# Kernel optimization log

Hardware: AMD Instinct MI355X
Metric: run time of the kernel (lower is better)

The kernel has to match this reference:

```python
import jax, jax.numpy as jnp
import numpy as np

N_NODES = 100000
N_EDGES = 3200000
NUM_FEATURES = 256
HIDDEN = 16
NUM_CLASSES = 40


def gcn_conv(x, edge_index, W, b, num_nodes):
    """PyG GCNConv: linear -> add self-loops -> symmetric deg norm -> scatter-add -> bias."""
    x = x @ W  # [N, out]
    loop = jnp.arange(num_nodes)
    src = jnp.concatenate([edge_index[0], loop])  # messages flow src -> dst
    dst = jnp.concatenate([edge_index[1], loop])
    # degree of target nodes (with self-loops)
    deg = jax.ops.segment_sum(jnp.ones_like(dst, dtype=x.dtype), dst,
                              num_segments=num_nodes)
    dinv = jnp.where(deg > 0, jax.lax.rsqrt(deg), 0.0)
    norm = dinv[src] * dinv[dst]  # [E+N]
    out = jax.ops.segment_sum(x[src] * norm[:, None], dst,
                              num_segments=num_nodes)
    return out + b


def setup_inputs() -> dict:
    key = jax.random.key(0)
    k1, k2, k3, k4 = jax.random.split(key, 4)
    x = jax.random.normal(k1, (N_NODES, NUM_FEATURES), dtype=jnp.float32)
    edge_index = jax.random.randint(k2, (2, N_EDGES), 0, N_NODES, dtype=jnp.int64)
    W1 = jax.random.normal(k3, (NUM_FEATURES, HIDDEN), dtype=jnp.float32) / np.sqrt(NUM_FEATURES)
    b1 = jnp.zeros((HIDDEN,), dtype=jnp.float32)
    W2 = jax.random.normal(k4, (HIDDEN, NUM_CLASSES), dtype=jnp.float32) / np.sqrt(HIDDEN)
    b2 = jnp.zeros((NUM_CLASSES,), dtype=jnp.float32)
    return {"x": x, "edge_index": edge_index, "W1": W1, "b1": b1, "W2": W2, "b2": b2}


def reference(x, edge_index, W1, b1, W2, b2):
    h = jax.nn.relu(gcn_conv(x, edge_index, W1, b1, N_NODES))
    return gcn_conv(h, edge_index, W2, b2, N_NODES)
```

## Files before the change

### kernel.cpp

```cpp
#include <hip/hip_runtime.h>
#include <hip/hip_fp16.h>

#define N_NODES   100000
#define N_EDGES   3200000
#define F_IN      256
#define HID       16
#define NCLS      40

#define CHUNK     8192
#define NCHK      ((N_EDGES + CHUNK - 1) / CHUNK)
#define GRID1     392
#define B2SHIFT   9
#define NB2       ((N_NODES + 511) >> B2SHIFT)
#define BCAP      17408

__global__ __launch_bounds__(128) void k1_all(const int* __restrict__ ei,
                                              const float* __restrict__ x,
                                              const float* __restrict__ W1,
                                              int* __restrict__ gcnt,
                                              int* __restrict__ buf,
                                              __half* __restrict__ y1h) {
    __shared__ float W1s[F_IN * HID];
    int* h   = (int*)W1s;
    int* cur = ((int*)W1s) + 256;
    int blk = blockIdx.x, t = threadIdx.x;

    if (blk < NCHK) {
        for (int j = t; j < NB2; j += 128) h[j] = 0;
        __syncthreads();
        int e0 = blk * CHUNK;
        int eN = min(CHUNK, N_EDGES - e0);
        const int4* d4 = (const int4*)(ei + N_EDGES + e0);
        const int4* s4 = (const int4*)(ei + e0);
        for (int i = t; i < (eN >> 2); i += 128) {
            int4 d = d4[i];
            atomicAdd(&h[d.x >> B2SHIFT], 1);
            atomicAdd(&h[d.y >> B2SHIFT], 1);
            atomicAdd(&h[d.z >> B2SHIFT], 1);
            atomicAdd(&h[d.w >> B2SHIFT], 1);
        }
        __syncthreads();
        for (int j = t; j < NB2; j += 128)
            cur[j] = j * BCAP + atomicAdd(&gcnt[j], h[j]);
        __syncthreads();
        for (int i = t; i < (eN >> 2); i += 128) {
            int4 d = d4[i], s = s4[i];
            int p0 = atomicAdd(&cur[d.x >> B2SHIFT], 1); buf[p0] = ((d.x & 511) << 17) | s.x;
            int p1 = atomicAdd(&cur[d.y >> B2SHIFT], 1); buf[p1] = ((d.y & 511) << 17) | s.y;
            int p2 = atomicAdd(&cur[d.z >> B2SHIFT], 1); buf[p2] = ((d.z & 511) << 17) | s.z;
            int p3 = atomicAdd(&cur[d.w >> B2SHIFT], 1); buf[p3] = ((d.w & 511) << 17) | s.w;
        }
        __syncthreads();
    }

    for (int i = t; i < F_IN * HID; i += 128) W1s[i] = W1[i];
    __syncthreads();

    int n0 = blk * 256 + t;
    int n1 = n0 + 128;
    if (n0 >= N_NODES) return;
    bool v1 = (n1 < N_NODES);

    const float4* xr0 = (const float4*)(x + (size_t)n0 * F_IN);
    const float4* xr1 = (const float4*)(x + (size_t)(v1 ? n1 : n0) * F_IN);
    float acc0[HID], acc1[HID];
    #pragma unroll
    for (int j = 0; j < HID; j++) { acc0[j] = 0.f; acc1[j] = 0.f; }

    #pragma unroll 2
    for (int k4 = 0; k4 < F_IN / 4; k4++) {
        float4 xa = xr0[k4];
        float4 xb = xr1[k4];
        int k = k4 * 4;
        #pragma unroll
        for (int hh = 0; hh < HID; hh++) {
            float w0 = W1s[(k + 0) * HID + hh];
            float w1 = W1s[(k + 1) * HID + hh];
            float w2 = W1s[(k + 2) * HID + hh];
            float w3 = W1s[(k + 3) * HID + hh];
            acc0[hh] += xa.x * w0 + xa.y * w1 + xa.z * w2 + xa.w * w3;
            acc1[hh] += xb.x * w0 + xb.y * w1 + xb.z * w2 + xb.w * w3;
        }
    }
    {
        __half2 hp[8];
        #pragma unroll
        for (int j = 0; j < 8; j++)
            hp[j] = __float22half2_rn(make_float2(acc0[2 * j], acc0[2 * j + 1]));
        float4* o = (float4*)(y1h + (size_t)n0 * HID);
        o[0] = ((float4*)hp)[0];
        o[1] = ((float4*)hp)[1];
    }
    if (v1) {
        __half2 hp[8];
        #pragma unroll
        for (int j = 0; j < 8; j++)
            hp[j] = __float22half2_rn(make_float2(acc1[2 * j], acc1[2 * j + 1]));
        float4* o = (float4*)(y1h + (size_t)n1 * HID);
        o[0] = ((float4*)hp)[0];
        o[1] = ((float4*)hp)[1];
    }
}

__global__ __launch_bounds__(512) void k3_build(const int* __restrict__ buf,
                                               const int* __restrict__ gcnt,
                                               int* __restrict__ rowptr,
                                               float* __restrict__ dinv,
                                               int* __restrict__ csr_src,
                                               __half* __restrict__ y1h) {
    __shared__ int lbuf[BCAP];
    __shared__ int hist[512], offs[512], cur[512];
    __shared__ int sc[256];
    __shared__ int s_base, s_cnt;
    int b = blockIdx.x, t = threadIdx.x;

    int cntv = 0;
    if (t < 256) { cntv = (t < NB2) ? gcnt[t] : 0; sc[t] = cntv; }
    hist[t] = 0;
    __syncthreads();
    for (int off = 1; off < 256; off <<= 1) {
        int u = 0;
        if (t < 256 && t >= off) u = sc[t - off];
        __syncthreads();
        if (t < 256) sc[t] += u;
        __syncthreads();
    }
    if (t == b) { s_base = sc[b] - cntv; s_cnt = cntv; }
    __syncthreads();
    int base = s_base, cnt = s_cnt;
    int src0 = b * BCAP;

    for (int i = t; i < cnt; i += 512) {
        int v = buf[src0 + i];
        if (i < BCAP) lbuf[i] = v;
        atomicAdd(&hist[v >> 17], 1);
    }
    __syncthreads();
    int v = hist[t];
    offs[t] = v;
    __syncthreads();
    for (int off = 1; off < 512; off <<= 1) {
        int u = (t >= off) ? offs[t - off] : 0;
        __syncthreads();
        offs[t] += u;
        __syncthreads();
    }
    int ex = offs[t] - v;
    int n = (b << B2SHIFT) + t;
    if (n < N_NODES) {
        rowptr[n] = base + ex;
        float dv = rsqrtf((float)(v + 1));
        dinv[n] = dv;
        float4* yr = (float4*)(y1h + (size_t)n * HID);
        float4 a = yr[0], bq = yr[1];
        __half2* ah = (__half2*)&a;
        __half2* bh = (__half2*)&bq;
        #pragma unroll
        for (int j = 0; j < 4; j++) {
            float2 fa = __half22float2(ah[j]);
            float2 fb = __half22float2(bh[j]);
            ah[j] = __float22half2_rn(make_float2(fa.x * dv, fa.y * dv));
            bh[j] = __float22half2_rn(make_float2(fb.x * dv, fb.y * dv));
        }
        yr[0] = a;
        yr[1] = bq;
    }
    if (b == 0 && t == 0) rowptr[N_NODES] = N_EDGES;
    cur[t] = ex;
    __syncthreads();
    for (int i = t; i < cnt; i += 512) {
        int p = (i < BCAP) ? lbuf[i] : buf[src0 + i];
        int pos = atomicAdd(&cur[p >> 17], 1);
        csr_src[base + pos] = p & 0x1FFFF;
    }
}

__device__ __forceinline__ void acc_row(const float4* __restrict__ tab, int s, float* acc) {
    float4 v0 = tab[(size_t)s * 2 + 0];
    float4 v1 = tab[(size_t)s * 2 + 1];
    const __half2* a0 = (const __half2*)&v0;
    const __half2* a1 = (const __half2*)&v1;
    #pragma unroll
    for (int j = 0; j < 4; j++) {
        float2 f0 = __half22float2(a0[j]);
        float2 f1 = __half22float2(a1[j]);
        acc[2 * j]         += f0.x;
        acc[2 * j + 1]     += f0.y;
        acc[8 + 2 * j]     += f1.x;
        acc[8 + 2 * j + 1] += f1.y;
    }
}

__device__ __forceinline__ void acc_row2(const float4* __restrict__ tab, int s0, int s1, float* acc) {
    float4 v0 = tab[(size_t)s0 * 2 + 0];
    float4 v1 = tab[(size_t)s0 * 2 + 1];
    float4 v2 = tab[(size_t)s1 * 2 + 0];
    float4 v3 = tab[(size_t)s1 * 2 + 1];
    const __half2* a0 = (const __half2*)&v0;
    const __half2* a1 = (const __half2*)&v1;
    const __half2* b0 = (const __half2*)&v2;
    const __half2* b1 = (const __half2*)&v3;
    #pragma unroll
    for (int j = 0; j < 4; j++) {
        float2 f0 = __half22float2(a0[j]);
        float2 f1 = __half22float2(a1[j]);
        float2 g0 = __half22float2(b0[j]);
        float2 g1 = __half22float2(b1[j]);
        acc[2 * j]         += f0.x + g0.x;
        acc[2 * j + 1]     += f0.y + g0.y;
        acc[8 + 2 * j]     += f1.x + g1.x;
        acc[8 + 2 * j + 1] += f1.y + g1.y;
    }
}

__global__ __launch_bounds__(256) void gather1_kernel(const int* __restrict__ rowptr,
                                                      const int* __restrict__ csr_src,
                                                      const __half* __restrict__ y1h,
                                                      const float* __restrict__ b1,
                                                      const float* __restrict__ dinv,
                                                      __half* __restrict__ zh) {
    int n   = blockIdx.x * 64 + (threadIdx.x >> 2);
    int sub = threadIdx.x & 3;
    if (n >= N_NODES) return;
    const float4* tab = (const float4*)y1h;
    int beg = rowptr[n], end = rowptr[n + 1];
    float acc[16];
    #pragma unroll
    for (int i = 0; i < 16; i++) acc[i] = 0.f;
    if (sub == 0) acc_row(tab, n, acc);
    int e = beg + sub;
    for (; e + 4 < end; e += 8)
        acc_row2(tab, csr_src[e], csr_src[e + 4], acc);
    if (e < end) acc_row(tab, csr_src[e], acc);
    #pragma unroll
    for (int m = 1; m < 4; m <<= 1) {
        #pragma unroll
        for (int i = 0; i < 16; i++) acc[i] += __shfl_xor(acc[i], m, 4);
    }
    if (sub < 2) {
        float dvn = dinv[n];
        const float4* b1q = (const float4*)b1;
        float4 ba = b1q[sub * 2], bb = b1q[sub * 2 + 1];
        float bv[8] = {ba.x, ba.y, ba.z, ba.w, bb.x, bb.y, bb.z, bb.w};
        __half2 outp[4];
        #pragma unroll
        for (int j = 0; j < 4; j++) {
            float2 r;
            r.x = fmaxf(dvn * acc[sub * 8 + 2 * j]     + bv[2 * j],     0.f) * dvn;
            r.y = fmaxf(dvn * acc[sub * 8 + 2 * j + 1] + bv[2 * j + 1], 0.f) * dvn;
            outp[j] = __float22half2_rn(r);
        }
        *(float4*)(zh + (size_t)n * HID + sub * 8) = *(float4*)outp;
    }
}

__global__ __launch_bounds__(256) void gather2_kernel(const int* __restrict__ rowptr,
                                                      const int* __restrict__ csr_src,
                                                      const __half* __restrict__ zh,
                                                      const float* __restrict__ W2,
                                                      const float* __restrict__ b2,
                                                      const float* __restrict__ dinv,
                                                      float* __restrict__ out) {
    __shared__ float W2s[HID * NCLS];
    __shared__ float b2s[NCLS];
    int t = threadIdx.x;
    for (int i = t; i < HID * NCLS; i += 256) W2s[i] = W2[i];
    if (t < NCLS) b2s[t] = b2[t];
    __syncthreads();

    int n   = blockIdx.x * 64 + (t >> 2);
    int sub = t & 3;
    if (n >= N_NODES) return;
    const float4* tab = (const float4*)zh;
    int beg = rowptr[n], end = rowptr[n + 1];
    float acc[16];
    #pragma unroll
    for (int i = 0; i < 16; i++) acc[i] = 0.f;
    if (sub == 0) acc_row(tab, n, acc);
    int e = beg + sub;
    for (; e + 4 < end; e += 8)
        acc_row2(tab, csr_src[e], csr_src[e + 4], acc);
    if (e < end) acc_row(tab, csr_src[e], acc);
    #pragma unroll
    for (int m = 1; m < 4; m <<= 1) {
        #pragma unroll
        for (int i = 0; i < 16; i++) acc[i] += __shfl_xor(acc[i], m, 4);
    }
    float dv = dinv[n];
    int c0 = sub * 10;
    float o[10];
    #pragma unroll
    for (int j = 0; j < 10; j++) o[j] = 0.f;
    #pragma unroll
    for (int h = 0; h < HID; h++) {
        float a = acc[h];
        const float* w = &W2s[h * NCLS + c0];
        #pragma unroll
        for (int j = 0; j < 10; j++) o[j] += a * w[j];
    }
    float* op = out + (size_t)n * NCLS + c0;
    #pragma unroll
    for (int j = 0; j < 5; j++) {
        float2 r = make_float2(dv * o[2 * j]     + b2s[c0 + 2 * j],
                               dv * o[2 * j + 1] + b2s[c0 + 2 * j + 1]);
        *(float2*)(op + 2 * j) = r;
    }
}

extern "C" void kernel_launch(void* const* d_in, const int* in_sizes, int n_in,
                              void* d_out, int out_size, void* d_ws, size_t ws_size,
                              hipStream_t stream) {
    const float* x   = (const float*)d_in[0];
    const int*   ei  = (const int*)  d_in[1];
    const float* W1  = (const float*)d_in[2];
    const float* b1  = (const float*)d_in[3];
    const float* W2  = (const float*)d_in[4];
    const float* b2  = (const float*)d_in[5];
    float* out = (float*)d_out;

    char* ws = (char*)d_ws;
    size_t off = 0;
    int*   gcnt = (int*)(ws + off); off += (size_t)NB2 * 4;
    off = (off + 15) & ~(size_t)15;
    int*    rowptr  = (int*)   (ws + off); off += (size_t)(N_NODES + 1) * 4;
    off = (off + 15) & ~(size_t)15;
    float*  dinv    = (float*) (ws + off); off += (size_t)N_NODES * 4;
    int*    csr_src = (int*)   (ws + off); off += (size_t)N_EDGES * 4;
    int*    buf     = (int*)   (ws + off); off += (size_t)NB2 * BCAP * 4;
    __half* y1h     = (__half*)(ws + off); off += (size_t)N_NODES * HID * 2;
    __half* zh      = (__half*)(ws + off); off += (size_t)N_NODES * HID * 2;

    hipMemsetAsync(gcnt, 0, (size_t)NB2 * 4, stream);
    k1_all   <<<GRID1, 128, 0, stream>>>(ei, x, W1, gcnt, buf, y1h);
    k3_build <<<NB2, 512, 0, stream>>>(buf, gcnt, rowptr, dinv, csr_src, y1h);
    gather1_kernel<<<(N_NODES + 63) / 64, 256, 0, stream>>>(rowptr, csr_src, y1h, b1, dinv, zh);
    gather2_kernel<<<(N_NODES + 63) / 64, 256, 0, stream>>>(rowptr, csr_src, zh, W2, b2, dinv, out);
}
```

Baseline: 333.3 us.

## Restructure GCN pipeline: global-atomic degrees, fuse CSR build with layer-1 gather

Degree counting moves to global atomics inside the GEMM kernel. Binning and the dinv scaling of y1 move into a new second kernel. The CSR build kernel now also does the layer-1 gather, using a per-bucket sorted source list held in LDS, so the separate gather1 launch and the dinv array go away. Layer 2 recomputes dinv from the rowptr difference. In exchange, the edge list is read an extra time, 3.2M global atomics hit deg, and the fused gather runs one thread per node with only 196 blocks, which may be poorly balanced.

```diff
diff --git a/kernel.cpp b/kernel.cpp
--- a/kernel.cpp
+++ b/kernel.cpp
@@ -7,57 +7,37 @@
 #define HID       16
 #define NCLS      40
 
-#define CHUNK     8192
-#define NCHK      ((N_EDGES + CHUNK - 1) / CHUNK)
-#define GRID1     392
+#define CHUNK     16384
+#define NBLK      ((N_EDGES + CHUNK - 1) / CHUNK)
 #define B2SHIFT   9
 #define NB2       ((N_NODES + 511) >> B2SHIFT)
 #define BCAP      17408
 
-__global__ __launch_bounds__(128) void k1_all(const int* __restrict__ ei,
-                                              const float* __restrict__ x,
-                                              const float* __restrict__ W1,
-                                              int* __restrict__ gcnt,
-                                              int* __restrict__ buf,
-                                              __half* __restrict__ y1h) {
+__global__ __launch_bounds__(256) void k1_gemm_deg(const int* __restrict__ ei,
+                                                   const float* __restrict__ x,
+                                                   const float* __restrict__ W1,
+                                                   int* __restrict__ deg,
+                                                   __half* __restrict__ y1h) {
     __shared__ float W1s[F_IN * HID];
-    int* h   = (int*)W1s;
-    int* cur = ((int*)W1s) + 256;
     int blk = blockIdx.x, t = threadIdx.x;
 
-    if (blk < NCHK) {
-        for (int j = t; j < NB2; j += 128) h[j] = 0;
-        __syncthreads();
-        int e0 = blk * CHUNK;
-        int eN = min(CHUNK, N_EDGES - e0);
-        const int4* d4 = (const int4*)(ei + N_EDGES + e0);
-        const int4* s4 = (const int4*)(ei + e0);
-        for (int i = t; i < (eN >> 2); i += 128) {
-            int4 d = d4[i];
-            atomicAdd(&h[d.x >> B2SHIFT], 1);
-            atomicAdd(&h[d.y >> B2SHIFT], 1);
-            atomicAdd(&h[d.z >> B2SHIFT], 1);
-            atomicAdd(&h[d.w >> B2SHIFT], 1);
-        }
-        __syncthreads();
-        for (int j = t; j < NB2; j += 128)
-            cur[j] = j * BCAP + atomicAdd(&gcnt[j], h[j]);
-        __syncthreads();
-        for (int i = t; i < (eN >> 2); i += 128) {
-            int4 d = d4[i], s = s4[i];
-            int p0 = atomicAdd(&cur[d.x >> B2SHIFT], 1); buf[p0] = ((d.x & 511) << 17) | s.x;
-            int p1 = atomicAdd(&cur[d.y >> B2SHIFT], 1); buf[p1] = ((d.y & 511) << 17) | s.y;
-            int p2 = atomicAdd(&cur[d.z >> B2SHIFT], 1); buf[p2] = ((d.z & 511) << 17) | s.z;
-            int p3 = atomicAdd(&cur[d.w >> B2SHIFT], 1); buf[p3] = ((d.w & 511) << 17) | s.w;
-        }
-        __syncthreads();
-    }
-
-    for (int i = t; i < F_IN * HID; i += 128) W1s[i] = W1[i];
-    __syncthreads();
-
-    int n0 = blk * 256 + t;
-    int n1 = n0 + 128;
+    #pragma unroll
+    for (int i = 0; i < (F_IN * HID) / 256; i++) W1s[t + i * 256] = W1[t + i * 256];
+
+    int e0 = blk * CHUNK;
+    int eN = min(CHUNK, N_EDGES - e0);
+    const int4* d4 = (const int4*)(ei + N_EDGES + e0);
+    for (int i = t; i < (eN >> 2); i += 256) {
+        int4 d = d4[i];
+        atomicAdd(&deg[d.x], 1);
+        atomicAdd(&deg[d.y], 1);
+        atomicAdd(&deg[d.z], 1);
+        atomicAdd(&deg[d.w], 1);
+    }
+    __syncthreads();
+
+    int n0 = blk * 512 + t;
+    int n1 = n0 + 256;
     if (n0 >= N_NODES) return;
     bool v1 = (n1 < N_NODES);
 
@@ -102,55 +82,17 @@
     }
 }
 
-__global__ __launch_bounds__(512) void k3_build(const int* __restrict__ buf,
-                                               const int* __restrict__ gcnt,
-                                               int* __restrict__ rowptr,
-                                               float* __restrict__ dinv,
-                                               int* __restrict__ csr_src,
-                                               __half* __restrict__ y1h) {
-    __shared__ int lbuf[BCAP];
-    __shared__ int hist[512], offs[512], cur[512];
-    __shared__ int sc[256];
-    __shared__ int s_base, s_cnt;
-    int b = blockIdx.x, t = threadIdx.x;
-
-    int cntv = 0;
-    if (t < 256) { cntv = (t < NB2) ? gcnt[t] : 0; sc[t] = cntv; }
-    hist[t] = 0;
-    __syncthreads();
-    for (int off = 1; off < 256; off <<= 1) {
-        int u = 0;
-        if (t < 256 && t >= off) u = sc[t - off];
-        __syncthreads();
-        if (t < 256) sc[t] += u;
-        __syncthreads();
-    }
-    if (t == b) { s_base = sc[b] - cntv; s_cnt = cntv; }
-    __syncthreads();
-    int base = s_base, cnt = s_cnt;
-    int src0 = b * BCAP;
-
-    for (int i = t; i < cnt; i += 512) {
-        int v = buf[src0 + i];
-        if (i < BCAP) lbuf[i] = v;
-        atomicAdd(&hist[v >> 17], 1);
-    }
-    __syncthreads();
-    int v = hist[t];
-    offs[t] = v;
-    __syncthreads();
-    for (int off = 1; off < 512; off <<= 1) {
-        int u = (t >= off) ? offs[t - off] : 0;
-        __syncthreads();
-        offs[t] += u;
-        __syncthreads();
-    }
-    int ex = offs[t] - v;
-    int n = (b << B2SHIFT) + t;
+__global__ __launch_bounds__(512) void k2_scale_bin(const int* __restrict__ ei,
+                                                    const int* __restrict__ deg,
+                                                    __half* __restrict__ y1h,
+                                                    int* __restrict__ gcnt,
+                                                    int* __restrict__ buf) {
+    __shared__ int h[NB2], cur[NB2];
+    int blk = blockIdx.x, t = threadIdx.x;
+
+    int n = blk * 512 + t;
     if (n < N_NODES) {
-        rowptr[n] = base + ex;
-        float dv = rsqrtf((float)(v + 1));
-        dinv[n] = dv;
+        float dv = rsqrtf((float)(deg[n] + 1));
         float4* yr = (float4*)(y1h + (size_t)n * HID);
         float4 a = yr[0], bq = yr[1];
         __half2* ah = (__half2*)&a;
@@ -165,13 +107,30 @@
         yr[0] = a;
         yr[1] = bq;
     }
-    if (b == 0 && t == 0) rowptr[N_NODES] = N_EDGES;
-    cur[t] = ex;
-    __syncthreads();
-    for (int i = t; i < cnt; i += 512) {
-        int p = (i < BCAP) ? lbuf[i] : buf[src0 + i];
-        int pos = atomicAdd(&cur[p >> 17], 1);
-        csr_src[base + pos] = p & 0x1FFFF;
+
+    for (int j = t; j < NB2; j += 512) h[j] = 0;
+    __syncthreads();
+    int e0 = blk * CHUNK;
+    int eN = min(CHUNK, N_EDGES - e0);
+    const int4* s4 = (const int4*)(ei + e0);
+    const int4* d4 = (const int4*)(ei + N_EDGES + e0);
+    for (int i = t; i < (eN >> 2); i += 512) {
+        int4 d = d4[i];
+        atomicAdd(&h[d.x >> B2SHIFT], 1);
+        atomicAdd(&h[d.y >> B2SHIFT], 1);
+        atomicAdd(&h[d.z >> B2SHIFT], 1);
+        atomicAdd(&h[d.w >> B2SHIFT], 1);
+    }
+    __syncthreads();
+    for (int j = t; j < NB2; j += 512)
+        cur[j] = j * BCAP + atomicAdd(&gcnt[j], h[j]);
+    __syncthreads();
+    for (int i = t; i < (eN >> 2); i += 512) {
+        int4 d = d4[i], s = s4[i];
+        int p0 = atomicAdd(&cur[d.x >> B2SHIFT], 1); buf[p0] = ((d.x & 511) << 17) | s.x;
+        int p1 = atomicAdd(&cur[d.y >> B2SHIFT], 1); buf[p1] = ((d.y & 511) << 17) | s.y;
+        int p2 = atomicAdd(&cur[d.z >> B2SHIFT], 1); buf[p2] = ((d.z & 511) << 17) | s.z;
+        int p3 = atomicAdd(&cur[d.w >> B2SHIFT], 1); buf[p3] = ((d.w & 511) << 17) | s.w;
     }
 }
 
@@ -213,16 +172,106 @@
     }
 }
 
-__global__ __launch_bounds__(256) void gather1_kernel(const int* __restrict__ rowptr,
+__global__ __launch_bounds__(512) void k3_build_gather(const int* __restrict__ buf,
+                                                       const int* __restrict__ gcnt,
+                                                       int* __restrict__ rowptr,
+                                                       int* __restrict__ csr_src,
+                                                       const __half* __restrict__ y1h,
+                                                       const float* __restrict__ b1,
+                                                       __half* __restrict__ zh) {
+    __shared__ int lsorted[BCAP];
+    __shared__ int hist[512], offs[512], cur[512];
+    __shared__ int sc[256];
+    __shared__ float b1s[HID];
+    __shared__ int s_base, s_cnt;
+    int b = blockIdx.x, t = threadIdx.x;
+
+    if (t < HID) b1s[t] = b1[t];
+    int cntv = 0;
+    if (t < 256) { cntv = (t < NB2) ? gcnt[t] : 0; sc[t] = cntv; }
+    hist[t] = 0;
+    __syncthreads();
+    for (int off = 1; off < 256; off <<= 1) {
+        int u = 0;
+        if (t < 256 && t >= off) u = sc[t - off];
+        __syncthreads();
+        if (t < 256) sc[t] += u;
+        __syncthreads();
+    }
+    if (t == b) { s_base = sc[b] - cntv; s_cnt = cntv; }
+    __syncthreads();
+    int base = s_base, cnt = s_cnt;
+    int src0 = b * BCAP;
+
+    for (int i = t; i < cnt; i += 512)
+        atomicAdd(&hist[buf[src0 + i] >> 17], 1);
+    __syncthreads();
+    int v = hist[t];
+    offs[t] = v;
+    __syncthreads();
+    for (int off = 1; off < 512; off <<= 1) {
+        int u = (t >= off) ? offs[t - off] : 0;
+        __syncthreads();
+        offs[t] += u;
+        __syncthreads();
+    }
+    int ex = offs[t] - v;
+    int n = (b << B2SHIFT) + t;
+    if (n < N_NODES) rowptr[n] = base + ex;
+    if (b == 0 && t == 0) rowptr[N_NODES] = N_EDGES;
+    cur[t] = ex;
+    __syncthreads();
+    for (int i = t; i < cnt; i += 512) {
+        int p = buf[src0 + i];
+        int pos = atomicAdd(&cur[p >> 17], 1);
+        int s = p & 0x1FFFF;
+        csr_src[base + pos] = s;
+        lsorted[pos] = s;
+    }
+    __syncthreads();
+
+    if (n < N_NODES) {
+        const float4* tab = (const float4*)y1h;
+        float acc[16];
+        #pragma unroll
+        for (int i = 0; i < 16; i++) acc[i] = 0.f;
+        acc_row(tab, n, acc);
+        int e = ex, endv = ex + v;
+        for (; e + 1 < endv; e += 2)
+            acc_row2(tab, lsorted[e], lsorted[e + 1], acc);
+        if (e < endv) acc_row(tab, lsorted[e], acc);
+        float dv = rsqrtf((float)(v + 1));
+        __half2 outp[8];
+        #pragma unroll
+        for (int j = 0; j < 8; j++) {
+            float2 r;
+            r.x = fmaxf(dv * acc[2 * j]     + b1s[2 * j],     0.f) * dv;
+            r.y = fmaxf(dv * acc[2 * j + 1] + b1s[2 * j + 1], 0.f) * dv;
+            outp[j] = __float22half2_rn(r);
+        }
+        float4* o = (float4*)(zh + (size_t)n * HID);
+        o[0] = ((float4*)outp)[0];
+        o[1] = ((float4*)outp)[1];
+    }
+}
+
+__global__ __launch_bounds__(256) void gather2_kernel(const int* __restrict__ rowptr,
                                                       const int* __restrict__ csr_src,
-                                                      const __half* __restrict__ y1h,
-                                                      const float* __restrict__ b1,
-                                                      const float* __restrict__ dinv,
-                                                      __half* __restrict__ zh) {
-    int n   = blockIdx.x * 64 + (threadIdx.x >> 2);
-    int sub = threadIdx.x & 3;
+                                                      const __half* __restrict__ zh,
+                                                      const float* __restrict__ W2,
+                                                      const float* __restrict__ b2,
+                                                      float* __restrict__ out) {
+    __shared__ float W2s[HID * NCLS];
+    __shared__ float b2s[NCLS];
+    int t = threadIdx.x;
+    for (int i = t; i < HID * NCLS; i += 256) W2s[i] = W2[i];
+    if (t < NCLS) b2s[t] = b2[t];
+    __syncthreads();
+
+    int n   = blockIdx.x * 64 + (t >> 2);
+    int sub = t & 3;
     if (n >= N_NODES) return;
-    const float4* tab = (const float4*)y1h;
+    const float4* tab = (const float4*)zh;
     int beg = rowptr[n], end = rowptr[n + 1];
     float acc[16];
     #pragma unroll
@@ -237,56 +286,7 @@
         #pragma unroll
         for (int i = 0; i < 16; i++) acc[i] += __shfl_xor(acc[i], m, 4);
     }
-    if (sub < 2) {
-        float dvn = dinv[n];
-        const float4* b1q = (const float4*)b1;
-        float4 ba = b1q[sub * 2], bb = b1q[sub * 2 + 1];
-        float bv[8] = {ba.x, ba.y, ba.z, ba.w, bb.x, bb.y, bb.z, bb.w};
-        __half2 outp[4];
-        #pragma unroll
-        for (int j = 0; j < 4; j++) {
-            float2 r;
-            r.x = fmaxf(dvn * acc[sub * 8 + 2 * j]     + bv[2 * j],     0.f) * dvn;
-            r.y = fmaxf(dvn * acc[sub * 8 + 2 * j + 1] + bv[2 * j + 1], 0.f) * dvn;
-            outp[j] = __float22half2_rn(r);
-        }
-        *(float4*)(zh + (size_t)n * HID + sub * 8) = *(float4*)outp;
-    }
-}
-
-__global__ __launch_bounds__(256) void gather2_kernel(const int* __restrict__ rowptr,
-                                                      const int* __restrict__ csr_src,
-                                                      const __half* __restrict__ zh,
-                                                      const float* __restrict__ W2,
-                                                      const float* __restrict__ b2,
-                                                      const float* __restrict__ dinv,
-                                                      float* __restrict__ out) {
-    __shared__ float W2s[HID * NCLS];
-    __shared__ float b2s[NCLS];
-    int t = threadIdx.x;
-    for (int i = t; i < HID * NCLS; i += 256) W2s[i] = W2[i];
-    if (t < NCLS) b2s[t] = b2[t];
-    __syncthreads();
-
-    int n   = blockIdx.x * 64 + (t >> 2);
-    int sub = t & 3;
-    if (n >= N_NODES) return;
-    const float4* tab = (const float4*)zh;
-    int beg = rowptr[n], end = rowptr[n + 1];
-    float acc[16];
-    #pragma unroll
-    for (int i = 0; i < 16; i++) acc[i] = 0.f;
-    if (sub == 0) acc_row(tab, n, acc);
-    int e = beg + sub;
-    for (; e + 4 < end; e += 8)
-        acc_row2(tab, csr_src[e], csr_src[e + 4], acc);
-    if (e < end) acc_row(tab, csr_src[e], acc);
-    #pragma unroll
-    for (int m = 1; m < 4; m <<= 1) {
-        #pragma unroll
-        for (int i = 0; i < 16; i++) acc[i] += __shfl_xor(acc[i], m, 4);
-    }
-    float dv = dinv[n];
+    float dv = rsqrtf((float)(end - beg + 1));
     int c0 = sub * 10;
     float o[10];
     #pragma unroll
@@ -320,19 +320,19 @@
 
     char* ws = (char*)d_ws;
     size_t off = 0;
+    int*   deg  = (int*)(ws + off); off += (size_t)N_NODES * 4;
     int*   gcnt = (int*)(ws + off); off += (size_t)NB2 * 4;
     off = (off + 15) & ~(size_t)15;
     int*    rowptr  = (int*)   (ws + off); off += (size_t)(N_NODES + 1) * 4;
     off = (off + 15) & ~(size_t)15;
-    float*  dinv    = (float*) (ws + off); off += (size_t)N_NODES * 4;
     int*    csr_src = (int*)   (ws + off); off += (size_t)N_EDGES * 4;
     int*    buf     = (int*)   (ws + off); off += (size_t)NB2 * BCAP * 4;
     __half* y1h     = (__half*)(ws + off); off += (size_t)N_NODES * HID * 2;
     __half* zh      = (__half*)(ws + off); off += (size_t)N_NODES * HID * 2;
 
-    hipMemsetAsync(gcnt, 0, (size_t)NB2 * 4, stream);
-    k1_all   <<<GRID1, 128, 0, stream>>>(ei, x, W1, gcnt, buf, y1h);
-    k3_build <<<NB2, 512, 0, stream>>>(buf, gcnt, rowptr, dinv, csr_src, y1h);
-    gather1_kernel<<<(N_NODES + 63) / 64, 256, 0, stream>>>(rowptr, csr_src, y1h, b1, dinv, zh);
-    gather2_kernel<<<(N_NODES + 63) / 64, 256, 0, stream>>>(rowptr, csr_src, zh, W2, b2, dinv, out);
-}
+    hipMemsetAsync(deg, 0, ((size_t)N_NODES + NB2) * 4, stream);
+    k1_gemm_deg   <<<NBLK, 256, 0, stream>>>(ei, x, W1, deg, y1h);
+    k2_scale_bin  <<<NBLK, 512, 0, stream>>>(ei, deg, y1h, gcnt, buf);
+    k3_build_gather<<<NB2, 512, 0, stream>>>(buf, gcnt, rowptr, csr_src, y1h, b1, zh);
+    gather2_kernel<<<(N_NODES + 63) / 64, 256, 0, stream>>>(rowptr, csr_src, zh, W2, b2, out);
+}
```

New measurement: 420.9 us. 1.26x slower.
